# Performance work log

Hardware: AMD Instinct MI355X
Metric: run time of the kernel (lower is better)

The kernel has to match this reference:

```python
import jax, jax.numpy as jnp
import numpy as np

# Model dims (match init_kwargs)
E = 512        # embed_dim
H = 8          # n_heads
L = 6          # n_layers
DFF = 2048     # PyTorch TransformerEncoderLayer default dim_feedforward
K = 1024       # codebook_size
V = 32         # num_joints
NQ = 1         # n_q
T = 64         # frames
B = 2
MAX_T = 512    # time_pos table size
LN_EPS = 1e-5


def make_block_causal_mask(t, v):
    """True=keep. Causal across frames, full attention within a frame."""
    s = t * v
    i = np.arange(s)
    tril = i[:, None] >= i[None, :]
    same_frame = (i[:, None] // v) == (i[None, :] // v)
    return jnp.asarray(tril | same_frame)


def setup_inputs() -> dict:
    key = jax.random.key(0)
    ks = jax.random.split(key, 20)
    sc = 0.02
    inp = {
        "indices": jax.random.randint(ks[0], (B, T, V, NQ), 0, K, dtype=jnp.int64 if jax.config.jax_enable_x64 else jnp.int32),
        "attention_mask": make_block_causal_mask(T, V),
        # embedding tables
        "code_emb": jax.random.normal(ks[1], (K, E), jnp.float32) * sc,
        "stage_emb": jax.random.normal(ks[2], (NQ, E), jnp.float32) * sc,
        "time_pos": jax.random.normal(ks[3], (MAX_T, E), jnp.float32) * sc,
        "joint_pos": jax.random.normal(ks[4], (V, E), jnp.float32) * sc,
        # per-layer stacked transformer params
        "in_proj_w": jax.random.normal(ks[5], (L, 3 * E, E), jnp.float32) * sc,
        "in_proj_b": jnp.zeros((L, 3 * E), jnp.float32),
        "out_w": jax.random.normal(ks[6], (L, E, E), jnp.float32) * sc,
        "out_b": jnp.zeros((L, E), jnp.float32),
        "ln1_g": jnp.ones((L, E), jnp.float32),
        "ln1_b": jnp.zeros((L, E), jnp.float32),
        "lin1_w": jax.random.normal(ks[7], (L, DFF, E), jnp.float32) * sc,
        "lin1_b": jnp.zeros((L, DFF), jnp.float32),
        "lin2_w": jax.random.normal(ks[8], (L, E, DFF), jnp.float32) * sc,
        "lin2_b": jnp.zeros((L, E), jnp.float32),
        "ln2_g": jnp.ones((L, E), jnp.float32),
        "ln2_b": jnp.zeros((L, E), jnp.float32),
    }
    return inp


def _ln(x, g, b):
    mu = jnp.mean(x, axis=-1, keepdims=True)
    var = jnp.mean(jnp.square(x - mu), axis=-1, keepdims=True)
    return (x - mu) * jax.lax.rsqrt(var + LN_EPS) * g + b


def _mha(x, keep, wi, bi, wo, bo):
    Bq, S, _ = x.shape
    dh = E // H
    qkv = x @ wi.T + bi                       # [B,S,3E]
    q, k, v = jnp.split(qkv, 3, axis=-1)
    q = q.reshape(Bq, S, H, dh)
    k = k.reshape(Bq, S, H, dh)
    v = v.reshape(Bq, S, H, dh)
    scores = jnp.einsum('bqhd,bkhd->bhqk', q, k) / jnp.sqrt(jnp.float32(dh))
    scores = jnp.where(keep[None, None], scores, jnp.float32(-1e30))
    attn = jax.nn.softmax(scores, axis=-1)
    o = jnp.einsum('bhqk,bkhd->bqhd', attn, v).reshape(Bq, S, E)
    return o @ wo.T + bo


def _transformer(indices, keep, code_emb, stage_emb, time_pos, joint_pos,
                 in_proj_w, in_proj_b, out_w, out_b, ln1_g, ln1_b,
                 lin1_w, lin1_b, lin2_w, lin2_b, ln2_g, ln2_b):
    Bq, Tq, Vq, nq = indices.shape
    emb = code_emb[indices] + stage_emb[None, None, None]       # [B,T,V,nq,E]
    emb = emb.reshape(Bq, Tq, Vq * nq, E)
    v_ids = jnp.repeat(jnp.arange(Vq), nq)
    emb = emb + time_pos[:Tq][None, :, None, :] + joint_pos[v_ids][None, None, :, :]
    x = emb.reshape(Bq, Tq * Vq * nq, E)
    for l in range(L):
        y = _ln(x, ln1_g[l], ln1_b[l])
        x = x + _mha(y, keep, in_proj_w[l], in_proj_b[l], out_w[l], out_b[l])
        y = _ln(x, ln2_g[l], ln2_b[l])
        h = jax.nn.gelu(y @ lin1_w[l].T + lin1_b[l], approximate=False)
        x = x + h @ lin2_w[l].T + lin2_b[l]
    return x.reshape(Bq, Tq, Vq * nq, E)


def reference(indices, attention_mask, code_emb, stage_emb, time_pos, joint_pos,
              in_proj_w, in_proj_b, out_w, out_b, ln1_g, ln1_b,
              lin1_w, lin1_b, lin2_w, lin2_b, ln2_g, ln2_b):
    # attention_mask is [T*V, T*V] with n_q=1, so no repeat_interleave needed.
    keep = attention_mask
    if NQ > 1 and attention_mask.shape[0] == T * V:
        keep = jnp.repeat(jnp.repeat(attention_mask, NQ, 0), NQ, 1)
    return _transformer(indices, keep, code_emb, stage_emb, time_pos, joint_pos,
                        in_proj_w, in_proj_b, out_w, out_b, ln1_g, ln1_b,
                        lin1_w, lin1_b, lin2_w, lin2_b, ln2_g, ln2_b)
```

## Files before the change

kernel.cpp:

```cpp
#include <hip/hip_runtime.h>
#include <hip/hip_bf16.h>
#include <math.h>

#define E 512
#define H_HEADS 8
#define DH 64
#define NLAYER 6
#define DFF 2048
#define SEQ 2048
#define NB 2
#define M_TOK (NB*SEQ)

typedef float f32x4_t __attribute__((ext_vector_type(4)));
typedef __bf16 bf16x8_t __attribute__((ext_vector_type(8)));
typedef short s16x8_t __attribute__((ext_vector_type(8)));

__device__ __forceinline__ short f2bf(float f) {
    union { float f; unsigned u; } v; v.f = f;
    unsigned r = v.u + 0x7FFFu + ((v.u >> 16) & 1u);
    return (short)(r >> 16);
}

__device__ __forceinline__ bf16x8_t mk_frag(short4 lo, short4 hi) {
    s16x8_t t;
    t[0] = lo.x; t[1] = lo.y; t[2] = lo.z; t[3] = lo.w;
    t[4] = hi.x; t[5] = hi.y; t[6] = hi.z; t[7] = hi.w;
    return __builtin_bit_cast(bf16x8_t, t);
}

__device__ __forceinline__ void gload16(const void* g, void* l) {
    __builtin_amdgcn_global_load_lds(
        (const __attribute__((address_space(1))) void*)g,
        (__attribute__((address_space(3))) void*)l, 16, 0, 0);
}

__global__ __launch_bounds__(256) void embed_kernel(
    const int* __restrict__ idx, const float* __restrict__ ce,
    const float* __restrict__ se, const float* __restrict__ tp,
    const float* __restrict__ jp, float* __restrict__ x)
{
    int i = blockIdx.x * 256 + threadIdx.x;
    int e4 = i & 127;
    int row = i >> 7;
    int v = row & 31;
    int t = (row >> 5) & 63;
    int code = idx[row];
    const float4* ce4 = (const float4*)ce;
    const float4* se4 = (const float4*)se;
    const float4* tp4 = (const float4*)tp;
    const float4* jp4 = (const float4*)jp;
    float4 a = ce4[code * 128 + e4];
    float4 b = se4[e4];
    float4 c = tp4[t * 128 + e4];
    float4 d = jp4[v * 128 + e4];
    float4 o;
    o.x = a.x + b.x + c.x + d.x;
    o.y = a.y + b.y + c.y + d.y;
    o.z = a.z + b.z + c.z + d.z;
    o.w = a.w + b.w + c.w + d.w;
    ((float4*)x)[i] = o;
}

__global__ __launch_bounds__(256) void cast4_kernel(
    const float* __restrict__ w0, const float* __restrict__ w1,
    const float* __restrict__ w2, const float* __restrict__ w3,
    short* __restrict__ o)
{
    int i = blockIdx.x * 256 + threadIdx.x;
    const float* src; int off;
    if (i < 98304)       { src = w0; off = i; }
    else if (i < 131072) { src = w1; off = i - 98304; }
    else if (i < 262144) { src = w2; off = i - 131072; }
    else                 { src = w3; off = i - 262144; }
    float4 a = ((const float4*)src)[off * 2];
    float4 b = ((const float4*)src)[off * 2 + 1];
    s16x8_t s;
    s[0] = f2bf(a.x); s[1] = f2bf(a.y); s[2] = f2bf(a.z); s[3] = f2bf(a.w);
    s[4] = f2bf(b.x); s[5] = f2bf(b.y); s[6] = f2bf(b.z); s[7] = f2bf(b.w);
    *(s16x8_t*)&o[(size_t)i * 8] = s;
}

__global__ __launch_bounds__(256) void ln_kernel(
    const float* __restrict__ x, short* __restrict__ y,
    const float* __restrict__ g, const float* __restrict__ b)
{
    int wave = threadIdx.x >> 6;
    int lane = threadIdx.x & 63;
    int row = blockIdx.x * 4 + wave;
    const float4* xr = (const float4*)(x + (size_t)row * E);
    float4 v0 = xr[lane];
    float4 v1 = xr[lane + 64];
    float s  = v0.x + v0.y + v0.z + v0.w + v1.x + v1.y + v1.z + v1.w;
    float ss = v0.x*v0.x + v0.y*v0.y + v0.z*v0.z + v0.w*v0.w
             + v1.x*v1.x + v1.y*v1.y + v1.z*v1.z + v1.w*v1.w;
    #pragma unroll
    for (int off = 32; off; off >>= 1) {
        s  += __shfl_xor(s, off, 64);
        ss += __shfl_xor(ss, off, 64);
    }
    float mu = s * (1.f / E);
    float var = ss * (1.f / E) - mu * mu;
    float rs = rsqrtf(var + 1e-5f);
    const float4* g4 = (const float4*)g;
    const float4* b4 = (const float4*)b;
    float4 gg = g4[lane], bb = b4[lane];
    short4 o;
    o.x = f2bf((v0.x - mu) * rs * gg.x + bb.x);
    o.y = f2bf((v0.y - mu) * rs * gg.y + bb.y);
    o.z = f2bf((v0.z - mu) * rs * gg.z + bb.z);
    o.w = f2bf((v0.w - mu) * rs * gg.w + bb.w);
    *(short4*)&y[(size_t)row * E + lane * 4] = o;
    gg = g4[lane + 64]; bb = b4[lane + 64];
    o.x = f2bf((v1.x - mu) * rs * gg.x + bb.x);
    o.y = f2bf((v1.y - mu) * rs * gg.y + bb.y);
    o.z = f2bf((v1.z - mu) * rs * gg.z + bb.z);
    o.w = f2bf((v1.w - mu) * rs * gg.w + bb.w);
    *(short4*)&y[(size_t)row * E + 256 + lane * 4] = o;
}

template<int MODE>
__global__ __launch_bounds__(256) void gemm_mfma_kernel(
    const short* __restrict__ A, const short* __restrict__ W,
    const float* __restrict__ bias, const float* __restrict__ res,
    void* __restrict__ out, int N, int K)
{
    __shared__ short As[128 * 64];
    __shared__ short Bs[128 * 64];
    int nb = N >> 7;
    int bx = blockIdx.x % nb;
    int by = blockIdx.x / nb;
    int tid = threadIdx.x;
    int lane = tid & 63, g = lane >> 4, l16 = lane & 15;
    int w = tid >> 6, wm = w >> 1, wn = w & 1;
    int wbase = tid & 192;

    f32x4_t acc[4][4] = {};
    const short* Ab = A + (size_t)(by * 128) * K;
    const short* Wb = W + (size_t)(bx * 128) * K;

    for (int k0 = 0; k0 < K; k0 += 64) {
        __syncthreads();
        #pragma unroll
        for (int u = 0; u < 4; ++u) {
            int c = u * 256 + tid;
            int row = c >> 3, c8 = c & 7;
            gload16(Ab + (size_t)row * K + k0 + c8 * 8, As + (u * 256 + wbase) * 8);
            gload16(Wb + (size_t)row * K + k0 + c8 * 8, Bs + (u * 256 + wbase) * 8);
        }
        __syncthreads();
        #pragma unroll
        for (int ks = 0; ks < 2; ++ks) {
            bf16x8_t af[4], bf[4];
            #pragma unroll
            for (int i = 0; i < 4; ++i) {
                af[i] = *(const bf16x8_t*)&As[(wm * 64 + i * 16 + l16) * 64 + ks * 32 + g * 8];
                bf[i] = *(const bf16x8_t*)&Bs[(wn * 64 + i * 16 + l16) * 64 + ks * 32 + g * 8];
            }
            #pragma unroll
            for (int mi = 0; mi < 4; ++mi)
                #pragma unroll
                for (int ni = 0; ni < 4; ++ni)
                    acc[mi][ni] = __builtin_amdgcn_mfma_f32_16x16x32_bf16(
                        af[mi], bf[ni], acc[mi][ni], 0, 0, 0);
        }
    }

    int gm0 = by * 128 + wm * 64;
    int gn0 = bx * 128 + wn * 64;
    #pragma unroll
    for (int ni = 0; ni < 4; ++ni) {
        int gn = gn0 + ni * 16 + l16;
        float bv = bias[gn];
        #pragma unroll
        for (int mi = 0; mi < 4; ++mi) {
            #pragma unroll
            for (int r = 0; r < 4; ++r) {
                int gm = gm0 + mi * 16 + g * 4 + r;
                float v = acc[mi][ni][r] + bv;
                if (MODE == 2) v = 0.5f * v * (1.f + erff(v * 0.70710678118f));
                if (MODE == 1) {
                    v += res[(size_t)gm * N + gn];
                    ((float*)out)[(size_t)gm * N + gn] = v;
                } else {
                    ((short*)out)[(size_t)gm * N + gn] = f2bf(v);
                }
            }
        }
    }
}

__global__ __launch_bounds__(256) void attn_mfma_kernel(
    const short* __restrict__ qkv, short* __restrict__ out)
{
    __shared__ __align__(16) short Qs[64 * 68];
    __shared__ __align__(16) short Ks[32 * 68];
    __shared__ __align__(16) short Vt[64 * 36];
    __shared__ __align__(16) float Ol[4 * 16 * 68];

    int qb = blockIdx.x & 31;
    int h  = (blockIdx.x >> 5) & 7;
    int b  = blockIdx.x >> 8;
    int tid  = threadIdx.x;
    int w    = tid >> 6;
    int lane = tid & 63;
    int g    = lane >> 4;
    int l16  = lane & 15;

    const short* base = qkv + (size_t)(b * SEQ) * 1536;

    #pragma unroll
    for (int u = 0; u < 4; ++u) {
        int f = tid + 256 * u;
        int qr = f >> 4, c4 = f & 15;
        short4 v = *(const short4*)(base + (size_t)(qb * 64 + qr) * 1536 + h * 64 + c4 * 4);
        *(short4*)&Qs[qr * 68 + c4 * 4] = v;
    }
    __syncthreads();

    bf16x8_t qf[2];
    #pragma unroll
    for (int ks = 0; ks < 2; ++ks) {
        const short* qrow = &Qs[(w * 16 + l16) * 68];
        short4 lo = *(const short4*)&qrow[4 * g + 32 * ks];
        short4 hi = *(const short4*)&qrow[4 * g + 16 + 32 * ks];
        qf[ks] = mk_frag(lo, hi);
    }

    f32x4_t oa[4] = {};
    float mrun = -1e30f, lrun = 0.f;

    int kend = qb * 64 + (w >> 1) * 32 + 32;
    int kmax = (qb + 1) * 64;

    for (int kt = 0; kt < kmax; kt += 32) {
        __syncthreads();
        #pragma unroll
        for (int u = 0; u < 2; ++u) {
            int f = tid + 256 * u;
            int key = f >> 4, c4 = f & 15;
            const short* row = base + (size_t)(kt + key) * 1536 + h * 64;
            short4 kv = *(const short4*)(row + 512 + c4 * 4);
            *(short4*)&Ks[key * 68 + c4 * 4] = kv;
            short4 vv = *(const short4*)(row + 1024 + c4 * 4);
            Vt[(c4 * 4 + 0) * 36 + key] = vv.x;
            Vt[(c4 * 4 + 1) * 36 + key] = vv.y;
            Vt[(c4 * 4 + 2) * 36 + key] = vv.z;
            Vt[(c4 * 4 + 3) * 36 + key] = vv.w;
        }
        __syncthreads();
        if (kt >= kend) continue;

        f32x4_t st[2];
        #pragma unroll
        for (int mt = 0; mt < 2; ++mt) {
            f32x4_t acc = {0.f, 0.f, 0.f, 0.f};
            #pragma unroll
            for (int ks = 0; ks < 2; ++ks) {
                const short* krow = &Ks[(mt * 16 + l16) * 68];
                short4 lo = *(const short4*)&krow[4 * g + 32 * ks];
                short4 hi = *(const short4*)&krow[4 * g + 16 + 32 * ks];
                acc = __builtin_amdgcn_mfma_f32_16x16x32_bf16(mk_frag(lo, hi), qf[ks], acc, 0, 0, 0);
            }
            st[mt] = acc;
        }

        float s8[8];
        #pragma unroll
        for (int mt = 0; mt < 2; ++mt)
            #pragma unroll
            for (int r = 0; r < 4; ++r)
                s8[mt * 4 + r] = st[mt][r] * 0.125f;
        float tm = s8[0];
        #pragma unroll
        for (int j = 1; j < 8; ++j) tm = fmaxf(tm, s8[j]);
        tm = fmaxf(tm, __shfl_xor(tm, 16));
        tm = fmaxf(tm, __shfl_xor(tm, 32));
        float mnew = fmaxf(mrun, tm);
        float c = __expf(mrun - mnew);
        mrun = mnew;
        float ps = 0.f;
        short pb[8];
        #pragma unroll
        for (int j = 0; j < 8; ++j) {
            float p = __expf(s8[j] - mrun);
            ps += p;
            pb[j] = f2bf(p);
        }
        ps += __shfl_xor(ps, 16);
        ps += __shfl_xor(ps, 32);
        lrun = lrun * c + ps;
        #pragma unroll
        for (int dt = 0; dt < 4; ++dt)
            #pragma unroll
            for (int r = 0; r < 4; ++r)
                oa[dt][r] *= c;
        s16x8_t pt;
        #pragma unroll
        for (int j = 0; j < 8; ++j) pt[j] = pb[j];
        bf16x8_t pf = __builtin_bit_cast(bf16x8_t, pt);

        #pragma unroll
        for (int dt = 0; dt < 4; ++dt) {
            const short* vrow = &Vt[(dt * 16 + l16) * 36];
            short4 lo = *(const short4*)&vrow[4 * g];
            short4 hi = *(const short4*)&vrow[16 + 4 * g];
            oa[dt] = __builtin_amdgcn_mfma_f32_16x16x32_bf16(mk_frag(lo, hi), pf, oa[dt], 0, 0, 0);
        }
    }

    float inv = 1.f / lrun;
    #pragma unroll
    for (int dt = 0; dt < 4; ++dt)
        #pragma unroll
        for (int r = 0; r < 4; ++r)
            Ol[(w * 16 + l16) * 68 + 16 * dt + 4 * g + r] = oa[dt][r] * inv;
    int qr = lane >> 2, cc = lane & 3;
    const float* orow = &Ol[(w * 16 + qr) * 68 + cc * 16];
    s16x8_t s0, s1;
    #pragma unroll
    for (int j = 0; j < 8; ++j) { s0[j] = f2bf(orow[j]); s1[j] = f2bf(orow[8 + j]); }
    size_t gb = (size_t)(b * SEQ + qb * 64 + w * 16 + qr) * E + h * 64 + cc * 16;
    *(s16x8_t*)&out[gb] = s0;
    *(s16x8_t*)&out[gb + 8] = s1;
}

extern "C" void kernel_launch(void* const* d_in, const int* in_sizes, int n_in,
                              void* d_out, int out_size, void* d_ws, size_t ws_size,
                              hipStream_t stream) {
    const int*   idx = (const int*)d_in[0];
    const float* ce  = (const float*)d_in[2];
    const float* se  = (const float*)d_in[3];
    const float* tp  = (const float*)d_in[4];
    const float* jp  = (const float*)d_in[5];
    const float* ipw = (const float*)d_in[6];
    const float* ipb = (const float*)d_in[7];
    const float* ow  = (const float*)d_in[8];
    const float* ob  = (const float*)d_in[9];
    const float* l1g = (const float*)d_in[10];
    const float* l1b = (const float*)d_in[11];
    const float* w1  = (const float*)d_in[12];
    const float* b1  = (const float*)d_in[13];
    const float* w2  = (const float*)d_in[14];
    const float* b2  = (const float*)d_in[15];
    const float* l2g = (const float*)d_in[16];
    const float* l2b = (const float*)d_in[17];

    float* x = (float*)d_out;
    short* y_bf   = (short*)d_ws;
    short* qkv_bf = (short*)((char*)d_ws + (4u << 20));
    short* h_bf   = qkv_bf;
    short* wb     = (short*)((char*)d_ws + (20u << 20));
    short* wip = wb;
    short* wob = wb + 786432;
    short* w1b = wb + 1048576;
    short* w2b = wb + 2097152;

    embed_kernel<<<2048, 256, 0, stream>>>(idx, ce, se, tp, jp, x);

    for (int l = 0; l < NLAYER; ++l) {
        cast4_kernel<<<1536, 256, 0, stream>>>(
            ipw + (size_t)l * 786432, ow + (size_t)l * 262144,
            w1 + (size_t)l * 1048576, w2 + (size_t)l * 1048576, wb);
        ln_kernel<<<1024, 256, 0, stream>>>(x, y_bf, l1g + l * E, l1b + l * E);
        gemm_mfma_kernel<0><<<32 * 12, 256, 0, stream>>>(
            y_bf, wip, ipb + (size_t)l * 1536, nullptr, qkv_bf, 1536, 512);
        attn_mfma_kernel<<<512, 256, 0, stream>>>(qkv_bf, y_bf);
        gemm_mfma_kernel<1><<<32 * 4, 256, 0, stream>>>(
            y_bf, wob, ob + (size_t)l * E, x, x, 512, 512);
        ln_kernel<<<1024, 256, 0, stream>>>(x, y_bf, l2g + l * E, l2b + l * E);
        gemm_mfma_kernel<2><<<32 * 16, 256, 0, stream>>>(
            y_bf, w1b, b1 + (size_t)l * DFF, nullptr, h_bf, 2048, 512);
        gemm_mfma_kernel<1><<<32 * 4, 256, 0, stream>>>(
            h_bf, w2b, b2 + (size_t)l * E, x, x, 512, 2048);
    }
}
```

Before: 1.234 ms.

## Retile attention to 32-query blocks with register prefetch of next K/V tile

The attention kernel now uses 128-thread blocks that each own one 32-row query tile, which is exactly one frame. Each block iterates keys only up to the end of its own frame, so no wave idles on skipped tiles. Blocks are launched with the heaviest (latest) query tiles first to balance the causal triangle. The next K/V tile is loaded into registers while the current one is written to shared memory, and s_setprio brackets the MFMA sections. This doubles the block count and reloads K/V once per 32 queries instead of per 64, trading some extra global traffic for better load balance and latency hiding.

```diff
diff --git a/kernel.cpp b/kernel.cpp
--- a/kernel.cpp
+++ b/kernel.cpp
@@ -189,17 +189,18 @@
     }
 }
 
-__global__ __launch_bounds__(256) void attn_mfma_kernel(
+__global__ __launch_bounds__(128) void attn_mfma_kernel(
     const short* __restrict__ qkv, short* __restrict__ out)
 {
-    __shared__ __align__(16) short Qs[64 * 68];
+    __shared__ __align__(16) short Qs[32 * 68];
     __shared__ __align__(16) short Ks[32 * 68];
     __shared__ __align__(16) short Vt[64 * 36];
-    __shared__ __align__(16) float Ol[4 * 16 * 68];
-
-    int qb = blockIdx.x & 31;
-    int h  = (blockIdx.x >> 5) & 7;
-    int b  = blockIdx.x >> 8;
+    __shared__ __align__(16) float Ol[2 * 16 * 68];
+
+    int bid = blockIdx.x;
+    int qb = 63 - (bid & 63);
+    int h  = (bid >> 6) & 7;
+    int b  = bid >> 9;
     int tid  = threadIdx.x;
     int w    = tid >> 6;
     int lane = tid & 63;
@@ -210,10 +211,21 @@
 
     #pragma unroll
     for (int u = 0; u < 4; ++u) {
-        int f = tid + 256 * u;
+        int f = tid + 128 * u;
         int qr = f >> 4, c4 = f & 15;
-        short4 v = *(const short4*)(base + (size_t)(qb * 64 + qr) * 1536 + h * 64 + c4 * 4);
+        short4 v = *(const short4*)(base + (size_t)(qb * 32 + qr) * 1536 + h * 64 + c4 * 4);
         *(short4*)&Qs[qr * 68 + c4 * 4] = v;
+    }
+
+    int kend = (qb + 1) * 32;
+    short4 kreg[4], vreg[4];
+    #pragma unroll
+    for (int u = 0; u < 4; ++u) {
+        int f = tid + 128 * u;
+        int key = f >> 4, c4 = f & 15;
+        const short* row = base + (size_t)key * 1536 + h * 64;
+        kreg[u] = *(const short4*)(row + 512 + c4 * 4);
+        vreg[u] = *(const short4*)(row + 1024 + c4 * 4);
     }
     __syncthreads();
 
@@ -229,28 +241,32 @@
     f32x4_t oa[4] = {};
     float mrun = -1e30f, lrun = 0.f;
 
-    int kend = qb * 64 + (w >> 1) * 32 + 32;
-    int kmax = (qb + 1) * 64;
-
-    for (int kt = 0; kt < kmax; kt += 32) {
+    for (int kt = 0; kt < kend; kt += 32) {
         __syncthreads();
         #pragma unroll
-        for (int u = 0; u < 2; ++u) {
-            int f = tid + 256 * u;
+        for (int u = 0; u < 4; ++u) {
+            int f = tid + 128 * u;
             int key = f >> 4, c4 = f & 15;
-            const short* row = base + (size_t)(kt + key) * 1536 + h * 64;
-            short4 kv = *(const short4*)(row + 512 + c4 * 4);
-            *(short4*)&Ks[key * 68 + c4 * 4] = kv;
-            short4 vv = *(const short4*)(row + 1024 + c4 * 4);
-            Vt[(c4 * 4 + 0) * 36 + key] = vv.x;
-            Vt[(c4 * 4 + 1) * 36 + key] = vv.y;
-            Vt[(c4 * 4 + 2) * 36 + key] = vv.z;
-            Vt[(c4 * 4 + 3) * 36 + key] = vv.w;
+            *(short4*)&Ks[key * 68 + c4 * 4] = kreg[u];
+            Vt[(c4 * 4 + 0) * 36 + key] = vreg[u].x;
+            Vt[(c4 * 4 + 1) * 36 + key] = vreg[u].y;
+            Vt[(c4 * 4 + 2) * 36 + key] = vreg[u].z;
+            Vt[(c4 * 4 + 3) * 36 + key] = vreg[u].w;
+        }
+        if (kt + 32 < kend) {
+            #pragma unroll
+            for (int u = 0; u < 4; ++u) {
+                int f = tid + 128 * u;
+                int key = f >> 4, c4 = f & 15;
+                const short* row = base + (size_t)(kt + 32 + key) * 1536 + h * 64;
+                kreg[u] = *(const short4*)(row + 512 + c4 * 4);
+                vreg[u] = *(const short4*)(row + 1024 + c4 * 4);
+            }
         }
         __syncthreads();
-        if (kt >= kend) continue;
 
         f32x4_t st[2];
+        __builtin_amdgcn_s_setprio(1);
         #pragma unroll
         for (int mt = 0; mt < 2; ++mt) {
             f32x4_t acc = {0.f, 0.f, 0.f, 0.f};
@@ -263,6 +279,7 @@
             }
             st[mt] = acc;
         }
+        __builtin_amdgcn_s_setprio(0);
 
         float s8[8];
         #pragma unroll
@@ -299,6 +316,7 @@
         for (int j = 0; j < 8; ++j) pt[j] = pb[j];
         bf16x8_t pf = __builtin_bit_cast(bf16x8_t, pt);
 
+        __builtin_amdgcn_s_setprio(1);
         #pragma unroll
         for (int dt = 0; dt < 4; ++dt) {
             const short* vrow = &Vt[(dt * 16 + l16) * 36];
@@ -306,6 +324,7 @@
             short4 hi = *(const short4*)&vrow[16 + 4 * g];
             oa[dt] = __builtin_amdgcn_mfma_f32_16x16x32_bf16(mk_frag(lo, hi), pf, oa[dt], 0, 0, 0);
         }
+        __builtin_amdgcn_s_setprio(0);
     }
 
     float inv = 1.f / lrun;
@@ -319,7 +338,7 @@
     s16x8_t s0, s1;
     #pragma unroll
     for (int j = 0; j < 8; ++j) { s0[j] = f2bf(orow[j]); s1[j] = f2bf(orow[8 + j]); }
-    size_t gb = (size_t)(b * SEQ + qb * 64 + w * 16 + qr) * E + h * 64 + cc * 16;
+    size_t gb = (size_t)(b * SEQ + qb * 32 + w * 16 + qr) * E + h * 64 + cc * 16;
     *(s16x8_t*)&out[gb] = s0;
     *(s16x8_t*)&out[gb + 8] = s1;
 }
@@ -364,7 +383,7 @@
         ln_kernel<<<1024, 256, 0, stream>>>(x, y_bf, l1g + l * E, l1b + l * E);
         gemm_mfma_kernel<0><<<32 * 12, 256, 0, stream>>>(
             y_bf, wip, ipb + (size_t)l * 1536, nullptr, qkv_bf, 1536, 512);
-        attn_mfma_kernel<<<512, 256, 0, stream>>>(qkv_bf, y_bf);
+        attn_mfma_kernel<<<1024, 128, 0, stream>>>(qkv_bf, y_bf);
         gemm_mfma_kernel<1><<<32 * 4, 256, 0, stream>>>(
             y_bf, wob, ob + (size_t)l * E, x, x, 512, 512);
         ln_kernel<<<1024, 256, 0, stream>>>(x, y_bf, l2g + l * E, l2b + l * E);
```

Result: no change. 1.231 ms (-0.3%).
